# Optimization experiments

Measured on AMD Instinct MI355X. Metric: run time of the kernel, lower is better.

The kernel has to match this reference:

```python
import jax, jax.numpy as jnp
import numpy as np

D_MODEL = 1024
NUM_HEADS = 16
HEAD_DIM = D_MODEL // NUM_HEADS
B, S = 4, 2048


def setup_inputs() -> dict:
    key = jax.random.key(0)
    ks = jax.random.split(key, 11)
    scale = 1.0 / np.sqrt(D_MODEL)
    return {
        "query": jax.random.normal(ks[0], (B, S, D_MODEL), jnp.float32),
        "key": jax.random.normal(ks[1], (B, S, D_MODEL), jnp.float32),
        "value": jax.random.normal(ks[2], (B, S, D_MODEL), jnp.float32),
        "Wq": jax.random.normal(ks[3], (D_MODEL, D_MODEL), jnp.float32) * scale,
        "bq": jnp.zeros((D_MODEL,), jnp.float32),
        "Wk": jax.random.normal(ks[4], (D_MODEL, D_MODEL), jnp.float32) * scale,
        "bk": jnp.zeros((D_MODEL,), jnp.float32),
        "Wv": jax.random.normal(ks[5], (D_MODEL, D_MODEL), jnp.float32) * scale,
        "bv": jnp.zeros((D_MODEL,), jnp.float32),
        "Wo": jax.random.normal(ks[6], (D_MODEL, D_MODEL), jnp.float32) * scale,
        "bo": jnp.zeros((D_MODEL,), jnp.float32),
    }


def reference(query, key, value, Wq, bq, Wk, bk, Wv, bv, Wo, bo):
    b = query.shape[0]
    # nn.Linear: x @ W.T + b; weights stored [out, in]
    def split_heads(x):
        return x.reshape(b, -1, NUM_HEADS, HEAD_DIM).transpose(0, 2, 1, 3)  # [b,h,s,d]
    q = split_heads(query @ Wq.T + bq)
    k = split_heads(key @ Wk.T + bk)
    v = split_heads(value @ Wv.T + bv)
    scores = jnp.einsum("bhqd,bhkd->bhqk", q, k) / np.sqrt(HEAD_DIM)
    weights = jax.nn.softmax(scores, axis=-1)
    out = jnp.einsum("bhqk,bhkd->bhqd", weights, v)
    out = out.transpose(0, 2, 1, 3).reshape(b, -1, D_MODEL)
    return out @ Wo.T + bo
```

## Files before the change

### kernel.cpp

```cpp
#include <hip/hip_runtime.h>

typedef __bf16 bf16;
typedef __bf16 bf16x4 __attribute__((ext_vector_type(4)));
typedef __bf16 bf16x8 __attribute__((ext_vector_type(8)));
typedef float f32x4 __attribute__((ext_vector_type(4)));

#define MFMA16(a, b, c) __builtin_amdgcn_mfma_f32_16x16x32_bf16((a), (b), (c), 0, 0, 0)

#define QSCALE 0.1803368808f

__device__ __forceinline__ void async_cp16(const bf16* g, bf16* l) {
    __builtin_amdgcn_global_load_lds((const __attribute__((address_space(1))) void*)g,
                                     (__attribute__((address_space(3))) void*)l, 16, 0, 0);
}

struct CvtArgs { const float* src[7]; bf16* dst[7]; };
__global__ void cvt_all(CvtArgs a) {
    int bx = blockIdx.x, t, off;
    if (bx < 12288) { t = bx >> 12;            off = bx & 4095; }
    else            { t = 3 + ((bx - 12288) >> 9); off = (bx - 12288) & 511; }
    size_t i = (size_t)off * 256 + threadIdx.x;
    const float4* p = (const float4*)(a.src[t] + i * 8);
    float4 x = p[0], y = p[1];
    bf16x8 o;
    o[0] = (bf16)x.x; o[1] = (bf16)x.y; o[2] = (bf16)x.z; o[3] = (bf16)x.w;
    o[4] = (bf16)y.x; o[5] = (bf16)y.y; o[6] = (bf16)y.z; o[7] = (bf16)y.w;
    *(bf16x8*)(a.dst[t] + i * 8) = o;
}

__device__ __forceinline__ void gemm256(
    const bf16* __restrict__ A, const bf16* __restrict__ W,
    const float* __restrict__ bias, void* __restrict__ Cout,
    int mode, int m0, int n0)
{
    __shared__ bf16 lds[81920];
    const int K = 1024;
    const int tid = threadIdx.x;
    const int lane = tid & 63, wave = tid >> 6;
    const int l15 = lane & 15, quad = lane >> 4;
    const int wm = wave >> 2, wn = wave & 3;

    f32x4 acc[8][4] = {};

    const int rA = tid >> 2;
    const int cg8 = ((tid & 3) ^ (rA & 3)) * 8;
    const bf16* Ag0 = A + (size_t)(m0 + rA) * K + cg8;
    const bf16* Ag1 = A + (size_t)(m0 + rA + 128) * K + cg8;
    const bf16* Bg0 = W + (size_t)(n0 + rA) * K + cg8;
    const bf16* Bg1 = W + (size_t)(n0 + rA + 128) * K + cg8;

    auto stage = [&](int u, int k0) {
        bf16* p = lds + u;
        async_cp16(Ag0 + k0, p + tid * 8);
        async_cp16(Ag1 + k0, p + (tid + 512) * 8);
        async_cp16(Bg0 + k0, p + 8192 + tid * 8);
        async_cp16(Bg1 + k0, p + 8192 + (tid + 512) * 8);
    };

    const int csw = (quad ^ (l15 & 3)) * 8;
    int afo[8], bfo[4];
#pragma unroll
    for (int mt = 0; mt < 8; ++mt) afo[mt] = (wm * 128 + mt * 16 + l15) * 32 + csw;
#pragma unroll
    for (int nt = 0; nt < 4; ++nt) bfo[nt] = 8192 + (wn * 64 + nt * 16 + l15) * 32 + csw;

    auto phase = [&](int cu, int su, int k0s, bool doStage, int vmsel) {
        bf16x8 af[8], bf[4];
#pragma unroll
        for (int mt = 0; mt < 8; ++mt) af[mt] = *(const bf16x8*)(lds + cu + afo[mt]);
#pragma unroll
        for (int nt = 0; nt < 4; ++nt) bf[nt] = *(const bf16x8*)(lds + cu + bfo[nt]);
        if (doStage) stage(su, k0s);
        __builtin_amdgcn_s_barrier();
        asm volatile("s_waitcnt lgkmcnt(0)" ::: "memory");
        __builtin_amdgcn_sched_barrier(0);
        __builtin_amdgcn_s_setprio(1);
#pragma unroll
        for (int mt = 0; mt < 8; ++mt)
#pragma unroll
            for (int nt = 0; nt < 4; ++nt)
                acc[mt][nt] = MFMA16(af[mt], bf[nt], acc[mt][nt]);
        __builtin_amdgcn_s_setprio(0);
        if (vmsel == 2)      asm volatile("s_waitcnt vmcnt(8)" ::: "memory");
        else if (vmsel == 1) asm volatile("s_waitcnt vmcnt(4)" ::: "memory");
        else if (vmsel == 0) asm volatile("s_waitcnt vmcnt(0)" ::: "memory");
        if (vmsel >= 0) __builtin_amdgcn_s_barrier();
    };

    int r0 = 0, r1 = 16384, r2 = 32768, r3 = 49152, r4 = 65536;
    auto rot = [&]() { int tmp = r0; r0 = r1; r1 = r2; r2 = r3; r3 = r4; r4 = tmp; };

    stage(r0, 0); stage(r1, 32); stage(r2, 64);
    asm volatile("s_waitcnt vmcnt(8)" ::: "memory");
    __builtin_amdgcn_s_barrier();

    for (int t = 0; t < 14; ++t) {
        phase(r0, r3, (2 * t + 3) * 32, true, 2); rot();
        phase(r0, r3, (2 * t + 4) * 32, true, 2); rot();
    }
    phase(r0, r3, 31 * 32, true, 2); rot();
    phase(r0, 0, 0, false, 1); rot();
    phase(r0, 0, 0, false, 0); rot();
    phase(r0, 0, 0, false, -1);

#pragma unroll
    for (int mt = 0; mt < 8; ++mt) {
#pragma unroll
        for (int nt = 0; nt < 4; ++nt) {
            int col = n0 + wn * 64 + nt * 16 + l15;
            float bcol = (mode == 2) ? 0.0f : bias[col];
#pragma unroll
            for (int r = 0; r < 4; ++r) {
                int row = m0 + wm * 128 + mt * 16 + quad * 4 + r;
                float val = acc[mt][nt][r];
                if (mode == 2) {
                    val += bias[row];
                    int bb = col >> 11, s = col & 2047;
                    int u = s & 31;
                    int sp = (s & ~31) | (((u >> 2) & 3) * 8 + (u >> 4) * 4 + (u & 3));
                    ((bf16*)Cout)[((size_t)(bb * 1024 + row) << 11) + sp] = (bf16)val;
                } else if (mode == 3) {
                    ((float*)Cout)[(size_t)row * 1024 + col] = val + bcol;
                } else {
                    val += bcol;
                    if (mode == 0) val *= QSCALE;
                    int bb = row >> 11, s = row & 2047, hh = col >> 6, d = col & 63;
                    ((bf16*)Cout)[(((size_t)(bb * 16 + hh) * 2048 + s) << 6) + d] = (bf16)val;
                }
            }
        }
    }
}

struct QkvArgs {
    const bf16* A[3];
    const bf16* W[3];
    const float* bias[3];
    bf16* out[3];
};

__global__ __launch_bounds__(512, 2) void qkv_gemm(QkvArgs t) {
    int bid = blockIdx.x;
    int idx = (bid & 7) * 48 + (bid >> 3);
    int z = idx >> 7, r = idx & 127;
    int m0, n0;
    if (z < 2) { m0 = (r >> 2) * 256; n0 = (r & 3) * 256; }
    else       { m0 = (r >> 5) * 256; n0 = (r & 31) * 256; }
    gemm256(t.A[z], t.W[z], t.bias[z], t.out[z], z, m0, n0);
}

__global__ __launch_bounds__(512, 2) void oproj_gemm(
    const bf16* __restrict__ A, const bf16* __restrict__ W,
    const float* __restrict__ bias, float* __restrict__ Cout) {
    int bid = blockIdx.x;
    int idx = (bid & 7) * 16 + (bid >> 3);
    gemm256(A, W, bias, Cout, 3, (idx >> 2) * 256, (idx & 3) * 256);
}

__global__ __launch_bounds__(256, 2) void attn_kernel(
    const bf16* __restrict__ Qh, const bf16* __restrict__ Kh,
    const bf16* __restrict__ Vtg, bf16* __restrict__ AO)
{
    __shared__ bf16 Kl[64 * 64];
    __shared__ bf16 Vl[64 * 64];

    const int tid = threadIdx.x;
    const int lane = tid & 63, wave = tid >> 6;
    const int l15 = lane & 15, quad = lane >> 4, l7 = l15 & 7;
    const int h = blockIdx.y, b = blockIdx.z;
    const size_t base = (size_t)(b * 16 + h) << 17;
    const int q0 = blockIdx.x * 256 + wave * 64;

    bf16x8 qf[4][2];
#pragma unroll
    for (int qt = 0; qt < 4; ++qt)
#pragma unroll
        for (int ks = 0; ks < 2; ++ks)
            qf[qt][ks] = *(const bf16x8*)(Qh + base + (q0 + qt * 16 + l15) * 64 + ks * 32 + quad * 8);

    f32x4 o[4][4] = {};
    float ls[4] = {};

    const int sr = tid >> 3;
    const int sc0 = ((tid & 7) ^ (sr & 7)) * 8;
    const int sr2 = sr + 32;

    for (int kt = 0; kt < 2048; kt += 64) {
        __syncthreads();
        async_cp16(Kh + base + (size_t)(kt + sr) * 64 + sc0, Kl + tid * 8);
        async_cp16(Kh + base + (size_t)(kt + sr2) * 64 + sc0, Kl + (tid + 256) * 8);
        async_cp16(Vtg + base + (size_t)sr * 2048 + kt + sc0, Vl + tid * 8);
        async_cp16(Vtg + base + (size_t)sr2 * 2048 + kt + sc0, Vl + (tid + 256) * 8);
        __syncthreads();

        bf16x8 kb[2][4];
#pragma unroll
        for (int ks = 0; ks < 2; ++ks)
#pragma unroll
            for (int ktile = 0; ktile < 4; ++ktile)
                kb[ks][ktile] = *(const bf16x8*)(Kl + (ktile * 16 + l15) * 64 + (((ks * 4 + quad) ^ l7) * 8));

        bf16x8 pf[4][2];
#pragma unroll
        for (int qt = 0; qt < 4; ++qt) {
            f32x4 sc[4] = {};
#pragma unroll
            for (int ks = 0; ks < 2; ++ks)
#pragma unroll
                for (int ktile = 0; ktile < 4; ++ktile)
                    sc[ktile] = MFMA16(kb[ks][ktile], qf[qt][ks], sc[ktile]);
            float sum = 0.0f;
#pragma unroll
            for (int kc = 0; kc < 2; ++kc) {
                bf16x8 pk;
#pragma unroll
                for (int t = 0; t < 2; ++t)
#pragma unroll
                    for (int r = 0; r < 4; ++r) {
                        float p = __builtin_amdgcn_exp2f(sc[kc * 2 + t][r]);
                        sum += p;
                        pk[t * 4 + r] = (bf16)p;
                    }
                pf[qt][kc] = pk;
            }
            ls[qt] += sum;
        }

        bf16x8 va[4][2];
#pragma unroll
        for (int dt = 0; dt < 4; ++dt)
#pragma unroll
            for (int kc = 0; kc < 2; ++kc)
                va[dt][kc] = *(const bf16x8*)(Vl + (dt * 16 + l15) * 64 + (((kc * 4 + quad) ^ l7) * 8));

#pragma unroll
        for (int dt = 0; dt < 4; ++dt)
#pragma unroll
            for (int qt = 0; qt < 4; ++qt)
#pragma unroll
                for (int kc = 0; kc < 2; ++kc)
                    o[dt][qt] = MFMA16(va[dt][kc], pf[qt][kc], o[dt][qt]);
    }

#pragma unroll
    for (int qt = 0; qt < 4; ++qt) {
        float l = ls[qt];
        l += __shfl_xor(l, 16, 64);
        l += __shfl_xor(l, 32, 64);
        float inv = 1.0f / l;
        size_t rb = ((size_t)(b * 2048 + q0 + qt * 16 + l15)) * 1024 + h * 64;
#pragma unroll
        for (int dt = 0; dt < 4; ++dt) {
            bf16x4 ov = {(bf16)(o[dt][qt][0] * inv), (bf16)(o[dt][qt][1] * inv),
                         (bf16)(o[dt][qt][2] * inv), (bf16)(o[dt][qt][3] * inv)};
            *(bf16x4*)(AO + rb + dt * 16 + quad * 4) = ov;
        }
    }
}

extern "C" void kernel_launch(void* const* d_in, const int* in_sizes, int n_in,
                              void* d_out, int out_size, void* d_ws, size_t ws_size,
                              hipStream_t stream) {
    const float* q  = (const float*)d_in[0];
    const float* k  = (const float*)d_in[1];
    const float* v  = (const float*)d_in[2];
    const float* Wq = (const float*)d_in[3];
    const float* bq = (const float*)d_in[4];
    const float* Wk = (const float*)d_in[5];
    const float* bk = (const float*)d_in[6];
    const float* Wv = (const float*)d_in[7];
    const float* bv = (const float*)d_in[8];
    const float* Wo = (const float*)d_in[9];
    const float* bo = (const float*)d_in[10];
    float* out = (float*)d_out;

    const size_t NX = (size_t)8192 * 1024;
    const size_t NW = (size_t)1024 * 1024;
    bf16* ws  = (bf16*)d_ws;
    bf16* Xq  = ws;
    bf16* Xk  = Xq + NX;
    bf16* Xv  = Xk + NX;
    bf16* Wqb = Xv + NX;
    bf16* Wkb = Wqb + NW;
    bf16* Wvb = Wkb + NW;
    bf16* Wob = Wvb + NW;
    bf16* Qh  = Wob + NW;
    bf16* Kh  = Qh + NX;
    bf16* Vt  = Kh + NX;
    bf16* AO  = Xq;

    CvtArgs ca;
    ca.src[0] = q;  ca.dst[0] = Xq;
    ca.src[1] = k;  ca.dst[1] = Xk;
    ca.src[2] = v;  ca.dst[2] = Xv;
    ca.src[3] = Wq; ca.dst[3] = Wqb;
    ca.src[4] = Wk; ca.dst[4] = Wkb;
    ca.src[5] = Wv; ca.dst[5] = Wvb;
    ca.src[6] = Wo; ca.dst[6] = Wob;
    cvt_all<<<14336, 256, 0, stream>>>(ca);

    QkvArgs t;
    t.A[0] = Xq;  t.W[0] = Wqb; t.bias[0] = bq; t.out[0] = Qh;
    t.A[1] = Xk;  t.W[1] = Wkb; t.bias[1] = bk; t.out[1] = Kh;
    t.A[2] = Wvb; t.W[2] = Xv;  t.bias[2] = bv; t.out[2] = Vt;
    qkv_gemm<<<384, 512, 0, stream>>>(t);

    attn_kernel<<<dim3(8, 16, 4), dim3(256, 1, 1), 0, stream>>>(Qh, Kh, Vt, AO);

    oproj_gemm<<<128, 512, 0, stream>>>(AO, Wob, bo, out);
}
```

Measured before the change: 365.4 us.

## Shrink GEMM pipeline to 4 LDS stages and use 128-tile output projection

```diff
diff --git a/kernel.cpp b/kernel.cpp
--- a/kernel.cpp
+++ b/kernel.cpp
@@ -33,7 +33,7 @@
     const float* __restrict__ bias, void* __restrict__ Cout,
     int mode, int m0, int n0)
 {
-    __shared__ bf16 lds[81920];
+    __shared__ bf16 lds[65536];
     const int K = 1024;
     const int tid = threadIdx.x;
     const int lane = tid & 63, wave = tid >> 6;
@@ -43,7 +43,7 @@
     f32x4 acc[8][4] = {};
 
     const int rA = tid >> 2;
-    const int cg8 = ((tid & 3) ^ (rA & 3)) * 8;
+    const int cg8 = (((tid & 3) - (rA >> 1)) & 3) * 8;
     const bf16* Ag0 = A + (size_t)(m0 + rA) * K + cg8;
     const bf16* Ag1 = A + (size_t)(m0 + rA + 128) * K + cg8;
     const bf16* Bg0 = W + (size_t)(n0 + rA) * K + cg8;
@@ -57,7 +57,7 @@
         async_cp16(Bg1 + k0, p + 8192 + (tid + 512) * 8);
     };
 
-    const int csw = (quad ^ (l15 & 3)) * 8;
+    const int csw = ((quad + (l15 >> 1)) & 3) * 8;
     int afo[8], bfo[4];
 #pragma unroll
     for (int mt = 0; mt < 8; ++mt) afo[mt] = (wm * 128 + mt * 16 + l15) * 32 + csw;
@@ -81,27 +81,28 @@
             for (int nt = 0; nt < 4; ++nt)
                 acc[mt][nt] = MFMA16(af[mt], bf[nt], acc[mt][nt]);
         __builtin_amdgcn_s_setprio(0);
-        if (vmsel == 2)      asm volatile("s_waitcnt vmcnt(8)" ::: "memory");
-        else if (vmsel == 1) asm volatile("s_waitcnt vmcnt(4)" ::: "memory");
+        if (vmsel == 1)      asm volatile("s_waitcnt vmcnt(4)" ::: "memory");
         else if (vmsel == 0) asm volatile("s_waitcnt vmcnt(0)" ::: "memory");
         if (vmsel >= 0) __builtin_amdgcn_s_barrier();
     };
 
-    int r0 = 0, r1 = 16384, r2 = 32768, r3 = 49152, r4 = 65536;
-    auto rot = [&]() { int tmp = r0; r0 = r1; r1 = r2; r2 = r3; r3 = r4; r4 = tmp; };
-
-    stage(r0, 0); stage(r1, 32); stage(r2, 64);
-    asm volatile("s_waitcnt vmcnt(8)" ::: "memory");
+    const int U0 = 0, U1 = 16384, U2 = 32768, U3 = 49152;
+
+    stage(U0, 0); stage(U1, 32);
+    asm volatile("s_waitcnt vmcnt(4)" ::: "memory");
     __builtin_amdgcn_s_barrier();
 
-    for (int t = 0; t < 14; ++t) {
-        phase(r0, r3, (2 * t + 3) * 32, true, 2); rot();
-        phase(r0, r3, (2 * t + 4) * 32, true, 2); rot();
-    }
-    phase(r0, r3, 31 * 32, true, 2); rot();
-    phase(r0, 0, 0, false, 1); rot();
-    phase(r0, 0, 0, false, 0); rot();
-    phase(r0, 0, 0, false, -1);
+    for (int t = 0; t < 7; ++t) {
+        const int kb = t * 128;
+        phase(U0, U2, kb + 64, true, 1);
+        phase(U1, U3, kb + 96, true, 1);
+        phase(U2, U0, kb + 128, true, 1);
+        phase(U3, U1, kb + 160, true, 1);
+    }
+    phase(U0, U2, 960, true, 1);
+    phase(U1, U3, 992, true, 1);
+    phase(U2, 0, 0, false, 0);
+    phase(U3, 0, 0, false, -1);
 
 #pragma unroll
     for (int mt = 0; mt < 8; ++mt) {
@@ -132,6 +133,83 @@
     }
 }
 
+__device__ __forceinline__ void gemm_core(
+    const bf16* __restrict__ A, const bf16* __restrict__ W,
+    const float* __restrict__ bias, void* __restrict__ Cout,
+    int mode, int m0, int n0)
+{
+    __shared__ bf16 As[128 * 64];
+    __shared__ bf16 Bs[128 * 64];
+    const int K = 1024;
+    const int tid = threadIdx.x;
+    const int lane = tid & 63, wave = tid >> 6;
+    const int l15 = lane & 15, quad = lane >> 4, l7 = l15 & 7;
+    const int wm = wave >> 1, wn = wave & 1;
+
+    f32x4 acc[4][4] = {};
+
+    const int rb = tid >> 3;
+    const int cg8 = ((tid & 7) ^ (rb & 7)) * 8;
+    const bf16* Ag = A + (size_t)(m0 + rb) * K + cg8;
+    const bf16* Wg = W + (size_t)(n0 + rb) * K + cg8;
+    bf16* Al = As + tid * 8;
+    bf16* Bl = Bs + tid * 8;
+
+    for (int k0 = 0; k0 < K; k0 += 64) {
+        __syncthreads();
+#pragma unroll
+        for (int j = 0; j < 4; ++j) {
+            async_cp16(Ag + k0 + (size_t)(j * 32) * K, Al + j * 2048);
+            async_cp16(Wg + k0 + (size_t)(j * 32) * K, Bl + j * 2048);
+        }
+        __syncthreads();
+
+#pragma unroll
+        for (int ks = 0; ks < 2; ++ks) {
+            bf16x8 af[4], bfr[4];
+#pragma unroll
+            for (int t = 0; t < 4; ++t) {
+                const int sw = ((ks * 4 + quad) ^ l7) * 8;
+                af[t]  = *(const bf16x8*)(As + (wm * 64 + t * 16 + l15) * 64 + sw);
+                bfr[t] = *(const bf16x8*)(Bs + (wn * 64 + t * 16 + l15) * 64 + sw);
+            }
+#pragma unroll
+            for (int mt = 0; mt < 4; ++mt)
+#pragma unroll
+                for (int nt = 0; nt < 4; ++nt)
+                    acc[mt][nt] = MFMA16(af[mt], bfr[nt], acc[mt][nt]);
+        }
+    }
+
+#pragma unroll
+    for (int mt = 0; mt < 4; ++mt) {
+#pragma unroll
+        for (int nt = 0; nt < 4; ++nt) {
+            int col = n0 + wn * 64 + nt * 16 + l15;
+            float bcol = (mode == 2) ? 0.0f : bias[col];
+#pragma unroll
+            for (int r = 0; r < 4; ++r) {
+                int row = m0 + wm * 64 + mt * 16 + quad * 4 + r;
+                float val = acc[mt][nt][r];
+                if (mode == 2) {
+                    val += bias[row];
+                    int bb = col >> 11, s = col & 2047;
+                    int u = s & 31;
+                    int sp = (s & ~31) | (((u >> 2) & 3) * 8 + (u >> 4) * 4 + (u & 3));
+                    ((bf16*)Cout)[((size_t)(bb * 1024 + row) << 11) + sp] = (bf16)val;
+                } else if (mode == 3) {
+                    ((float*)Cout)[(size_t)row * 1024 + col] = val + bcol;
+                } else {
+                    val += bcol;
+                    if (mode == 0) val *= QSCALE;
+                    int bb = row >> 11, s = row & 2047, hh = col >> 6, d = col & 63;
+                    ((bf16*)Cout)[(((size_t)(bb * 16 + hh) * 2048 + s) << 6) + d] = (bf16)val;
+                }
+            }
+        }
+    }
+}
+
 struct QkvArgs {
     const bf16* A[3];
     const bf16* W[3];
@@ -149,12 +227,10 @@
     gemm256(t.A[z], t.W[z], t.bias[z], t.out[z], z, m0, n0);
 }
 
-__global__ __launch_bounds__(512, 2) void oproj_gemm(
+__global__ __launch_bounds__(256) void oproj_gemm(
     const bf16* __restrict__ A, const bf16* __restrict__ W,
     const float* __restrict__ bias, float* __restrict__ Cout) {
-    int bid = blockIdx.x;
-    int idx = (bid & 7) * 16 + (bid >> 3);
-    gemm256(A, W, bias, Cout, 3, (idx >> 2) * 256, (idx & 3) * 256);
+    gemm_core(A, W, bias, Cout, 3, blockIdx.x * 128, blockIdx.y * 128);
 }
 
 __global__ __launch_bounds__(256, 2) void attn_kernel(
@@ -307,5 +383,5 @@
 
     attn_kernel<<<dim3(8, 16, 4), dim3(256, 1, 1), 0, stream>>>(Qh, Kh, Vt, AO);
 
-    oproj_gemm<<<128, 512, 0, stream>>>(AO, Wob, bo, out);
-}
+    oproj_gemm<<<dim3(64, 8), dim3(256, 1, 1), 0, stream>>>(AO, Wob, bo, out);
+}
```

Result: faster. 354.4 us (-3.0%).
